# Kernel tuning notes

Measured on AMD Instinct MI355X. Metric: run time of the kernel, lower is better.

Reference implementation:

```python
import jax, jax.numpy as jnp
import numpy as np

H = 2048      # hidden_size
NH = 16       # num attention heads
KVH = 4       # num kv heads (GQA)
D = 128       # head_dim
E = 32        # num experts
K = 4         # top-k experts per token
I = 768       # moe intermediate size
T = 1024      # num tokens (single prefill sequence)
EPS = 1e-6
THETA = 10000.0


def rmsnorm(x, w, eps=EPS):
    return x * jax.lax.rsqrt(jnp.mean(x * x, axis=-1, keepdims=True) + eps) * w


def rope_cos_sin(positions, dim, theta):
    inv_freq = 1.0 / (theta ** (jnp.arange(0, dim, 2, dtype=jnp.float32) / dim))
    freqs = positions.astype(jnp.float32)[:, None] * inv_freq[None, :]   # [T, D/2]
    emb = jnp.concatenate([freqs, freqs], axis=-1)                       # [T, D]
    return jnp.cos(emb), jnp.sin(emb)


def apply_rope(x, cos, sin):
    # x: [T, nH, D]; cos/sin: [T, D] -> neox style: cat(-x2, x1)
    x1, x2 = jnp.split(x, 2, axis=-1)
    x_rot = jnp.concatenate([-x2, x1], axis=-1)
    return cos[:, None, :] * x + sin[:, None, :] * x_rot


def setup_inputs() -> dict:
    key = jax.random.key(0)
    ks = jax.random.split(key, 8)
    s = 0.02
    return {
        "hidden_states": jax.random.normal(ks[0], (T, H), jnp.float32),
        "positions": jnp.arange(T, dtype=jnp.int32),
        "ln1_w": jnp.ones((H,), jnp.float32),
        "w_qkv": jax.random.normal(ks[1], ((NH + 2 * KVH) * D, H), jnp.float32) * s,
        "q_norm_w": jnp.ones((D,), jnp.float32),
        "k_norm_w": jnp.ones((D,), jnp.float32),
        "w_o": jax.random.normal(ks[2], (H, NH * D), jnp.float32) * s,
        "ln2_w": jnp.ones((H,), jnp.float32),
        "router_w": jax.random.normal(ks[3], (E, H), jnp.float32) * s,
        "w_gate": jax.random.normal(ks[4], (E, I, H), jnp.float32) * s,
        "w_up": jax.random.normal(ks[5], (E, I, H), jnp.float32) * s,
        "w_down": jax.random.normal(ks[6], (E, H, I), jnp.float32) * s,
    }


def decoder_layer(hidden_states, positions, ln1_w, w_qkv, q_norm_w, k_norm_w,
                  w_o, ln2_w, router_w, w_gate, w_up, w_down):
    # ---- attention block ----
    residual = hidden_states
    h = rmsnorm(hidden_states, ln1_w)

    qkv = h @ w_qkv.T                                      # [T, (NH+2*KVH)*D]
    q, k, v = jnp.split(qkv, [NH * D, (NH + KVH) * D], axis=-1)
    q = q.reshape(T, NH, D)
    k = k.reshape(T, KVH, D)
    v = v.reshape(T, KVH, D)

    # per-head RMSNorm on q and k (Qwen3 QK-norm)
    q = rmsnorm(q, q_norm_w)
    k = rmsnorm(k, k_norm_w)

    cos, sin = rope_cos_sin(positions, D, THETA)
    q = apply_rope(q, cos, sin)
    k = apply_rope(k, cos, sin)

    rep = NH // KVH
    k = jnp.repeat(k, rep, axis=1)                         # [T, NH, D]
    v = jnp.repeat(v, rep, axis=1)

    scale = D ** -0.5
    scores = jnp.einsum("qhd,khd->hqk", q, k) * scale      # [NH, T, T]
    causal = jnp.tril(jnp.ones((T, T), bool))
    scores = jnp.where(causal[None], scores, -1e30)
    probs = jax.nn.softmax(scores, axis=-1)
    attn = jnp.einsum("hqk,khd->qhd", probs, v).reshape(T, NH * D)
    attn_out = attn @ w_o.T                                # [T, H]

    hidden = residual + attn_out

    # ---- MoE block ----
    residual = hidden
    h = rmsnorm(hidden, ln2_w)

    logits = h @ router_w.T                                # [T, E]
    router_probs = jax.nn.softmax(logits, axis=-1)
    topk_w, topk_idx = jax.lax.top_k(router_probs, K)      # softmax-then-topk
    topk_w = topk_w / (jnp.sum(topk_w, axis=-1, keepdims=True) + 1e-20)

    # scatter top-k weights into a dense [T, E] combine matrix
    combine = jnp.zeros((T, E), h.dtype).at[
        jnp.arange(T)[:, None], topk_idx].add(topk_w)

    gate = jnp.einsum("th,eih->tei", h, w_gate)            # [T, E, I]
    up = jnp.einsum("th,eih->tei", h, w_up)
    act = jax.nn.silu(gate) * up
    moe_out = jnp.einsum("tei,ehi,te->th", act, w_down, combine)

    return residual + moe_out


def reference(hidden_states, positions, ln1_w, w_qkv, q_norm_w, k_norm_w,
              w_o, ln2_w, router_w, w_gate, w_up, w_down):
    return decoder_layer(hidden_states, positions, ln1_w, w_qkv, q_norm_w,
                         k_norm_w, w_o, ln2_w, router_w, w_gate, w_up, w_down)
```

## Files before the change

### kernel.cpp

```cpp
#include <hip/hip_runtime.h>

typedef __attribute__((ext_vector_type(4))) float f32x4;
typedef __attribute__((ext_vector_type(8))) __bf16 bf16x8;
typedef __attribute__((ext_vector_type(4))) __bf16 bf16x4;

__device__ __forceinline__ f32x4 mfma16(bf16x8 a, bf16x8 b, f32x4 c) {
  return __builtin_amdgcn_mfma_f32_16x16x32_bf16(a, b, c, 0, 0, 0);
}

__global__ __launch_bounds__(256) void rmsnorm_k(const float* __restrict__ x,
                                                 const float* __restrict__ w,
                                                 float* __restrict__ y,
                                                 __bf16* __restrict__ yb) {
  int t = blockIdx.x;
  const float* xr = x + (size_t)t * 2048;
  int d0 = threadIdx.x * 4;
  float4 v1 = *(const float4*)(xr + d0);
  float4 v2 = *(const float4*)(xr + 1024 + d0);
  float ss = v1.x*v1.x + v1.y*v1.y + v1.z*v1.z + v1.w*v1.w
           + v2.x*v2.x + v2.y*v2.y + v2.z*v2.z + v2.w*v2.w;
#pragma unroll
  for (int mk = 1; mk < 64; mk <<= 1) ss += __shfl_xor(ss, mk);
  __shared__ float red[4];
  if ((threadIdx.x & 63) == 0) red[threadIdx.x >> 6] = ss;
  __syncthreads();
  float tot = red[0] + red[1] + red[2] + red[3];
  float rs = rsqrtf(tot * (1.0f / 2048.0f) + 1e-6f);
  float* yr = y + (size_t)t * 2048;
  float4 w1 = *(const float4*)(w + d0);
  float4 w2 = *(const float4*)(w + 1024 + d0);
  float4 o1, o2;
  o1.x = v1.x*rs*w1.x; o1.y = v1.y*rs*w1.y; o1.z = v1.z*rs*w1.z; o1.w = v1.w*rs*w1.w;
  o2.x = v2.x*rs*w2.x; o2.y = v2.y*rs*w2.y; o2.z = v2.z*rs*w2.z; o2.w = v2.w*rs*w2.w;
  *(float4*)(yr + d0) = o1;
  *(float4*)(yr + 1024 + d0) = o2;
  if (yb) {
    bf16x4 b1, b2;
    b1[0] = (__bf16)o1.x; b1[1] = (__bf16)o1.y; b1[2] = (__bf16)o1.z; b1[3] = (__bf16)o1.w;
    b2[0] = (__bf16)o2.x; b2[1] = (__bf16)o2.y; b2[2] = (__bf16)o2.z; b2[3] = (__bf16)o2.w;
    *(bf16x4*)(yb + (size_t)t * 2048 + d0) = b1;
    *(bf16x4*)(yb + (size_t)t * 2048 + 1024 + d0) = b2;
  }
}

__global__ __launch_bounds__(256) void gemm3_k(const float* __restrict__ A,
                                               const float* __restrict__ B,
                                               const float* __restrict__ RESID,
                                               float* __restrict__ C, int N, int K) {
  __shared__ __align__(16) __bf16 smAh[128 * 40];
  __shared__ __align__(16) __bf16 smAl[128 * 40];
  __shared__ __align__(16) __bf16 smBh[64 * 40];
  __shared__ __align__(16) __bf16 smBl[64 * 40];
  const int m0 = blockIdx.x * 128, n0 = blockIdx.y * 64;
  const int tid = threadIdx.x, l = tid & 63, w = tid >> 6;
  const int wm = w >> 1, wn = w & 1;
  float4 ra[4], rb[2];
#pragma unroll
  for (int i = 0; i < 4; i++) {
    int c = tid + i * 256, row = c >> 3, k4 = c & 7;
    ra[i] = *(const float4*)(A + (size_t)(m0 + row) * K + k4 * 4);
  }
#pragma unroll
  for (int i = 0; i < 2; i++) {
    int c = tid + i * 256, row = c >> 3, k4 = c & 7;
    rb[i] = *(const float4*)(B + (size_t)(n0 + row) * K + k4 * 4);
  }
  f32x4 acc[4][2] = {};
  for (int kt = 0; kt < K; kt += 32) {
    __syncthreads();
#pragma unroll
    for (int i = 0; i < 4; i++) {
      int c = tid + i * 256, row = c >> 3, k4 = c & 7;
      bf16x4 hv, lv;
#pragma unroll
      for (int j = 0; j < 4; j++) {
        float f = ((const float*)&ra[i])[j];
        __bf16 h = (__bf16)f; hv[j] = h; lv[j] = (__bf16)(f - (float)h);
      }
      *(bf16x4*)(smAh + row * 40 + k4 * 4) = hv;
      *(bf16x4*)(smAl + row * 40 + k4 * 4) = lv;
    }
#pragma unroll
    for (int i = 0; i < 2; i++) {
      int c = tid + i * 256, row = c >> 3, k4 = c & 7;
      bf16x4 hv, lv;
#pragma unroll
      for (int j = 0; j < 4; j++) {
        float f = ((const float*)&rb[i])[j];
        __bf16 h = (__bf16)f; hv[j] = h; lv[j] = (__bf16)(f - (float)h);
      }
      *(bf16x4*)(smBh + row * 40 + k4 * 4) = hv;
      *(bf16x4*)(smBl + row * 40 + k4 * 4) = lv;
    }
    __syncthreads();
    if (kt + 32 < K) {
#pragma unroll
      for (int i = 0; i < 4; i++) {
        int c = tid + i * 256, row = c >> 3, k4 = c & 7;
        ra[i] = *(const float4*)(A + (size_t)(m0 + row) * K + kt + 32 + k4 * 4);
      }
#pragma unroll
      for (int i = 0; i < 2; i++) {
        int c = tid + i * 256, row = c >> 3, k4 = c & 7;
        rb[i] = *(const float4*)(B + (size_t)(n0 + row) * K + kt + 32 + k4 * 4);
      }
    }
    bf16x8 ah[4], al[4], bh[2], bl[2];
    const int ko = (l >> 4) * 8;
#pragma unroll
    for (int f = 0; f < 4; f++) {
      int ar = wm * 64 + f * 16 + (l & 15);
      ah[f] = *(const bf16x8*)(smAh + ar * 40 + ko);
      al[f] = *(const bf16x8*)(smAl + ar * 40 + ko);
    }
#pragma unroll
    for (int f = 0; f < 2; f++) {
      int br = wn * 32 + f * 16 + (l & 15);
      bh[f] = *(const bf16x8*)(smBh + br * 40 + ko);
      bl[f] = *(const bf16x8*)(smBl + br * 40 + ko);
    }
#pragma unroll
    for (int mf = 0; mf < 4; mf++)
#pragma unroll
      for (int nf = 0; nf < 2; nf++) {
        acc[mf][nf] = mfma16(ah[mf], bh[nf], acc[mf][nf]);
        acc[mf][nf] = mfma16(ah[mf], bl[nf], acc[mf][nf]);
        acc[mf][nf] = mfma16(al[mf], bh[nf], acc[mf][nf]);
      }
  }
#pragma unroll
  for (int mf = 0; mf < 4; mf++) {
    int row = m0 + wm * 64 + mf * 16 + ((l >> 4) << 2);
#pragma unroll
    for (int nf = 0; nf < 2; nf++) {
      int col = n0 + wn * 32 + nf * 16 + (l & 15);
#pragma unroll
      for (int r = 0; r < 4; r++) {
        float v = acc[mf][nf][r];
        if (RESID) v += RESID[(size_t)(row + r) * N + col];
        C[(size_t)(row + r) * N + col] = v;
      }
    }
  }
}

__global__ __launch_bounds__(128) void qkr_k(const float* __restrict__ qkv,
                                             const int* __restrict__ pos,
                                             const float* __restrict__ qw,
                                             const float* __restrict__ kw,
                                             __bf16* __restrict__ qh, __bf16* __restrict__ ql,
                                             __bf16* __restrict__ kh, __bf16* __restrict__ kl,
                                             __bf16* __restrict__ vh, __bf16* __restrict__ vl) {
  int hs = blockIdx.x, t = blockIdx.y, d = threadIdx.x;
  float x = qkv[(size_t)t * 3072 + hs * 128 + d];
  __shared__ float xs[128];
  __shared__ float red[2];
  float o;
  if (hs < 20) {
    float ss = x * x;
#pragma unroll
    for (int mk = 1; mk < 64; mk <<= 1) ss += __shfl_xor(ss, mk);
    if ((d & 63) == 0) red[d >> 6] = ss;
    __syncthreads();
    float rs = rsqrtf((red[0] + red[1]) * (1.0f / 128.0f) + 1e-6f);
    const float* w = (hs < 16) ? qw : kw;
    float xn = x * rs * w[d];
    xs[d] = xn;
    __syncthreads();
    int i = d & 63;
    float invf = (float)pow(10000.0, -(double)i / 64.0);
    float ang = (float)pos[t] * invf;
    float cf = (float)cos((double)ang);
    float sf = (float)sin((double)ang);
    float rot = (d < 64) ? -xs[d + 64] : xs[d - 64];
    o = cf * xn + sf * rot;
  } else {
    o = x;
  }
  __bf16 hi = (__bf16)o;
  __bf16 lo = (__bf16)(o - (float)hi);
  if (hs < 16) {
    size_t idx = ((size_t)hs * 1024 + t) * 128 + d;
    qh[idx] = hi; ql[idx] = lo;
  } else if (hs < 20) {
    size_t idx = ((size_t)(hs - 16) * 1024 + t) * 128 + d;
    kh[idx] = hi; kl[idx] = lo;
  } else {
    size_t idx = ((size_t)(hs - 20) * 1024 + t) * 128 + d;
    vh[idx] = hi; vl[idx] = lo;
  }
}

__global__ void vtrans_k(const __bf16* __restrict__ vh, const __bf16* __restrict__ vl,
                         __bf16* __restrict__ vhT, __bf16* __restrict__ vlT) {
  __shared__ __bf16 tile[32][33];
  int kv = blockIdx.z, t0 = blockIdx.x * 32, d0 = blockIdx.y * 32;
  int tx = threadIdx.x, ty = threadIdx.y;
  tile[ty][tx] = vh[((size_t)kv * 1024 + t0 + ty) * 128 + d0 + tx];
  __syncthreads();
  vhT[((size_t)kv * 128 + d0 + ty) * 1024 + t0 + tx] = tile[tx][ty];
  __syncthreads();
  tile[ty][tx] = vl[((size_t)kv * 1024 + t0 + ty) * 128 + d0 + tx];
  __syncthreads();
  vlT[((size_t)kv * 128 + d0 + ty) * 1024 + t0 + tx] = tile[tx][ty];
}

__global__ __launch_bounds__(256) void flash_k(const __bf16* __restrict__ qh, const __bf16* __restrict__ ql,
                                               const __bf16* __restrict__ kh, const __bf16* __restrict__ kl,
                                               const __bf16* __restrict__ vhT, const __bf16* __restrict__ vlT,
                                               float* __restrict__ attn) {
  constexpr int KH = 0, KL = 4352, VH = 8704, VL = 13824, PH = 18944, PL = 21504;
  __shared__ __align__(16) __bf16 sm[24064];
  const int qt = blockIdx.x, h = blockIdx.y;
  const int q0 = qt * 64, kvh = h >> 2;
  const int tid = threadIdx.x, l = tid & 63, w = tid >> 6;
  for (int c = tid; c < 1024; c += 256) {
    int row = c >> 4, dc = c & 15;
    size_t g = ((size_t)h * 1024 + q0 + row) * 128 + dc * 8;
    *(bf16x8*)(sm + row * 136 + dc * 8) = *(const bf16x8*)(qh + g);
    *(bf16x8*)(sm + 8704 + row * 136 + dc * 8) = *(const bf16x8*)(ql + g);
  }
  __syncthreads();
  bf16x8 fqh[4], fql[4];
  {
    int row = w * 16 + (l & 15);
    int ko = (l >> 4) * 8;
#pragma unroll
    for (int kk = 0; kk < 4; kk++) {
      fqh[kk] = *(const bf16x8*)(sm + row * 136 + kk * 32 + ko);
      fql[kk] = *(const bf16x8*)(sm + 8704 + row * 136 + kk * 32 + ko);
    }
  }
  f32x4 acc[8] = {};
  float m_run[4], l_run[4];
#pragma unroll
  for (int r = 0; r < 4; r++) { m_run[r] = -1e30f; l_run[r] = 0.0f; }
  const int ktiles = (q0 + 64) >> 5;
  for (int kt = 0; kt < ktiles; kt++) {
    const int k0 = kt * 32;
    __syncthreads();
    for (int c = tid; c < 512; c += 256) {
      int row = c >> 4, dc = c & 15;
      size_t g = ((size_t)kvh * 1024 + k0 + row) * 128 + dc * 8;
      *(bf16x8*)(sm + KH + row * 136 + dc * 8) = *(const bf16x8*)(kh + g);
      *(bf16x8*)(sm + KL + row * 136 + dc * 8) = *(const bf16x8*)(kl + g);
    }
    for (int c = tid; c < 512; c += 256) {
      int row = c >> 2, tc = c & 3;
      size_t g = ((size_t)kvh * 128 + row) * 1024 + k0 + tc * 8;
      *(bf16x8*)(sm + VH + row * 40 + tc * 8) = *(const bf16x8*)(vhT + g);
      *(bf16x8*)(sm + VL + row * 40 + tc * 8) = *(const bf16x8*)(vlT + g);
    }
    __syncthreads();
    f32x4 s[2] = {};
#pragma unroll
    for (int kk = 0; kk < 4; kk++) {
      int ko = kk * 32 + (l >> 4) * 8;
#pragma unroll
      for (int nf = 0; nf < 2; nf++) {
        int key = nf * 16 + (l & 15);
        bf16x8 bh_ = *(const bf16x8*)(sm + KH + key * 136 + ko);
        bf16x8 bl_ = *(const bf16x8*)(sm + KL + key * 136 + ko);
        s[nf] = mfma16(fqh[kk], bh_, s[nf]);
        s[nf] = mfma16(fqh[kk], bl_, s[nf]);
        s[nf] = mfma16(fql[kk], bh_, s[nf]);
      }
    }
    const float scale = 0.08838834764831845f;
    const bool need_mask = (k0 + 31 > q0);
    float p[2][4], alpha[4];
#pragma unroll
    for (int r = 0; r < 4; r++) {
      float s0 = s[0][r] * scale, s1 = s[1][r] * scale;
      if (need_mask) {
        int qi = q0 + w * 16 + ((l >> 4) << 2) + r;
        if (k0 + (l & 15) > qi) s0 = -1e30f;
        if (k0 + 16 + (l & 15) > qi) s1 = -1e30f;
      }
      float mt = fmaxf(s0, s1);
#pragma unroll
      for (int mk = 1; mk < 16; mk <<= 1) mt = fmaxf(mt, __shfl_xor(mt, mk));
      float mnew = fmaxf(m_run[r], mt);
      alpha[r] = expf(m_run[r] - mnew);
      float p0 = expf(s0 - mnew), p1 = expf(s1 - mnew);
      float rs = p0 + p1;
#pragma unroll
      for (int mk = 1; mk < 16; mk <<= 1) rs += __shfl_xor(rs, mk);
      l_run[r] = l_run[r] * alpha[r] + rs;
      m_run[r] = mnew;
      p[0][r] = p0; p[1][r] = p1;
    }
#pragma unroll
    for (int nf2 = 0; nf2 < 8; nf2++)
#pragma unroll
      for (int r = 0; r < 4; r++) acc[nf2][r] *= alpha[r];
    const int phb = PH + w * 640, plb = PL + w * 640;
#pragma unroll
    for (int nf = 0; nf < 2; nf++)
#pragma unroll
      for (int r = 0; r < 4; r++) {
        int row = ((l >> 4) << 2) + r, col = nf * 16 + (l & 15);
        __bf16 hi = (__bf16)p[nf][r];
        sm[phb + row * 40 + col] = hi;
        sm[plb + row * 40 + col] = (__bf16)(p[nf][r] - (float)hi);
      }
    bf16x8 aph = *(const bf16x8*)(sm + phb + (l & 15) * 40 + (l >> 4) * 8);
    bf16x8 apl = *(const bf16x8*)(sm + plb + (l & 15) * 40 + (l >> 4) * 8);
#pragma unroll
    for (int nf2 = 0; nf2 < 8; nf2++) {
      int drow = nf2 * 16 + (l & 15);
      bf16x8 bvh = *(const bf16x8*)(sm + VH + drow * 40 + (l >> 4) * 8);
      bf16x8 bvl = *(const bf16x8*)(sm + VL + drow * 40 + (l >> 4) * 8);
      acc[nf2] = mfma16(aph, bvh, acc[nf2]);
      acc[nf2] = mfma16(aph, bvl, acc[nf2]);
      acc[nf2] = mfma16(apl, bvh, acc[nf2]);
    }
  }
#pragma unroll
  for (int r = 0; r < 4; r++) {
    float inv = 1.0f / l_run[r];
    size_t t = q0 + w * 16 + ((l >> 4) << 2) + r;
#pragma unroll
    for (int nf2 = 0; nf2 < 8; nf2++)
      attn[t * 2048 + h * 128 + nf2 * 16 + (l & 15)] = acc[nf2][r] * inv;
  }
}

__global__ __launch_bounds__(256) void router_k(const float* __restrict__ h2,
                                                const float* __restrict__ rw,
                                                int* __restrict__ tidx, float* __restrict__ tw,
                                                int* __restrict__ counts) {
  int t = blockIdx.x;
  int e = threadIdx.x >> 3, sub = threadIdx.x & 7;
  const float* hrow = h2 + (size_t)t * 2048;
  const float* wrow = rw + (size_t)e * 2048;
  float acc = 0.0f;
  for (int d = sub * 4; d < 2048; d += 32) {
    float4 a = *(const float4*)(hrow + d);
    float4 b = *(const float4*)(wrow + d);
    acc += a.x * b.x + a.y * b.y + a.z * b.z + a.w * b.w;
  }
  acc += __shfl_xor(acc, 1); acc += __shfl_xor(acc, 2); acc += __shfl_xor(acc, 4);
  __shared__ float lg[32];
  if (sub == 0) lg[e] = acc;
  __syncthreads();
  if (threadIdx.x < 64) {
    int l = threadIdx.x;
    float v = (l < 32) ? lg[l] : -3e38f;
    float mx = v;
#pragma unroll
    for (int mk = 1; mk < 32; mk <<= 1) mx = fmaxf(mx, __shfl_xor(mx, mk));
    float ex = (l < 32) ? expf(v - mx) : 0.0f;
    float den = ex;
#pragma unroll
    for (int mk = 1; mk < 32; mk <<= 1) den += __shfl_xor(den, mk);
    float prob = ex / den;
    float pv = v;
    int sel_i[4]; float sel_w[4]; float wsum = 0.0f;
#pragma unroll
    for (int j = 0; j < 4; j++) {
      float m2 = pv;
#pragma unroll
      for (int mk = 1; mk < 32; mk <<= 1) m2 = fmaxf(m2, __shfl_xor(m2, mk));
      unsigned long long ball = __ballot((pv == m2) && (l < 32));
      int sel = __ffsll(ball) - 1;
      float ps = __shfl(prob, sel);
      sel_i[j] = sel; sel_w[j] = ps; wsum += ps;
      if (l == sel) pv = -3e38f;
    }
    if (l < 4) {
      tidx[t * 4 + l] = sel_i[l];
      tw[t * 4 + l] = sel_w[l] / (wsum + 1e-20f);
      atomicAdd(&counts[sel_i[l]], 1);
    }
  }
}

__global__ void zero_k(int* counts) { if (threadIdx.x < 32) counts[threadIdx.x] = 0; }

__global__ void scan_k(const int* __restrict__ counts, int* __restrict__ offs,
                       int* __restrict__ cursor, int* __restrict__ pair_e,
                       int* __restrict__ pair_mt) {
  int l = threadIdx.x;
  int c = (l < 32) ? counts[l] : 0;
  int x = c;
#pragma unroll
  for (int d = 1; d < 32; d <<= 1) {
    int y = __shfl_up(x, d);
    if (l >= d) x += y;
  }
  if (l < 32) { offs[l] = x - c; cursor[l] = 0; }
  if (l == 31) offs[32] = x;
  if (l == 0) {
    int n = 0;
    for (int e = 0; e < 32; e++) {
      int ce = counts[e];
      for (int m = 0; m * 128 < ce; m++) { pair_e[n] = e; pair_mt[n] = m; n++; }
    }
    for (; n < 64; n++) { pair_e[n] = -1; pair_mt[n] = 0; }
  }
}

__global__ __launch_bounds__(256) void scatter_k(const int* __restrict__ tidx,
                                                 const int* __restrict__ offs,
                                                 int* __restrict__ cursor,
                                                 int* __restrict__ row_of_slot,
                                                 int* __restrict__ tok_of_row) {
  int p = blockIdx.x * 256 + threadIdx.x;
  if (p >= 4096) return;
  int e = tidx[p];
  int pos = atomicAdd(&cursor[e], 1);
  int row = offs[e] + pos;
  row_of_slot[p] = row;
  tok_of_row[row] = p >> 2;
}

__global__ __launch_bounds__(256) void gateup_k(const __bf16* __restrict__ h2b,
                                                const float* __restrict__ wg,
                                                const float* __restrict__ wu,
                                                const int* __restrict__ counts,
                                                const int* __restrict__ offs,
                                                const int* __restrict__ tok_of_row,
                                                const int* __restrict__ pair_e,
                                                const int* __restrict__ pair_mt,
                                                float* __restrict__ gu) {
  const int p = blockIdx.y;
  const int e = pair_e[p];
  if (e < 0) return;
  const int mt = pair_mt[p];
  const int cnt = counts[e];
  const int j = blockIdx.x;
  const float* wsel = (j < 6) ? wg : wu;
  const int n0 = (j < 6 ? j : j - 6) * 128;
  const int gout = (j < 6) ? 0 : 768;
  __shared__ __align__(16) __bf16 smA0[128 * 72];
  __shared__ __align__(16) __bf16 smA1[128 * 72];
  __shared__ __align__(16) __bf16 smB0[128 * 72];
  __shared__ __align__(16) __bf16 smB1[128 * 72];
  __shared__ int toks[128];
  const int tid = threadIdx.x, l = tid & 63, w = tid >> 6;
  const int wm = w >> 1, wn = w & 1;
  if (tid < 128) {
    int r = mt * 128 + tid;
    toks[tid] = (r < cnt) ? tok_of_row[offs[e] + r] : tok_of_row[offs[e]];
  }
  __syncthreads();
  const float* we = wsel + (size_t)e * 768 * 2048;
  const __bf16* aS[4];
  int aD[4];
#pragma unroll
  for (int i = 0; i < 4; i++) {
    aS[i] = h2b + (size_t)toks[(tid >> 3) + 32 * i] * 2048 + (tid & 7) * 8;
    aD[i] = ((tid >> 3) + 32 * i) * 72 + (tid & 7) * 8;
  }
  const float* bS[8];
  int bD[8];
#pragma unroll
  for (int i = 0; i < 8; i++) {
    bS[i] = we + (size_t)(n0 + (tid >> 4) + 16 * i) * 2048 + (tid & 15) * 4;
    bD[i] = ((tid >> 4) + 16 * i) * 72 + (tid & 15) * 4;
  }

  bf16x8 raE[4], raO[4];
  float4 rbE[8], rbO[8];

#define GU_ISSUE_E(kt) do { _Pragma("unroll") \
  for (int i = 0; i < 4; i++) raE[i] = *(const bf16x8*)(aS[i] + (kt)); \
  _Pragma("unroll") \
  for (int i = 0; i < 8; i++) rbE[i] = *(const float4*)(bS[i] + (kt)); } while (0)
#define GU_ISSUE_O(kt) do { _Pragma("unroll") \
  for (int i = 0; i < 4; i++) raO[i] = *(const bf16x8*)(aS[i] + (kt)); \
  _Pragma("unroll") \
  for (int i = 0; i < 8; i++) rbO[i] = *(const float4*)(bS[i] + (kt)); } while (0)
#define CVT4(dst, src) do { bf16x4 hv_; _Pragma("unroll") \
  for (int q_ = 0; q_ < 4; q_++) hv_[q_] = (__bf16)((const float*)&(src))[q_]; \
  *(bf16x4*)(dst) = hv_; } while (0)
#define GU_WRITE_E(smA, smB) do { _Pragma("unroll") \
  for (int i = 0; i < 4; i++) *(bf16x8*)(smA + aD[i]) = raE[i]; \
  _Pragma("unroll") \
  for (int i = 0; i < 8; i++) CVT4(smB + bD[i], rbE[i]); } while (0)
#define GU_WRITE_O(smA, smB) do { _Pragma("unroll") \
  for (int i = 0; i < 4; i++) *(bf16x8*)(smA + aD[i]) = raO[i]; \
  _Pragma("unroll") \
  for (int i = 0; i < 8; i++) CVT4(smB + bD[i], rbO[i]); } while (0)

  GU_ISSUE_E(0);
  GU_ISSUE_O(64);
  GU_WRITE_E(smA0, smB0);
  __syncthreads();

  f32x4 acc[4][4] = {};
  const int afo = (wm * 64 + (l & 15)) * 72 + (l >> 4) * 8;
  const int bfo = (wn * 64 + (l & 15)) * 72 + (l >> 4) * 8;
#define GU_COMPUTE(smA, smB) do { _Pragma("unroll") \
  for (int kk = 0; kk < 2; kk++) { \
    bf16x8 af_[4], bf_[4]; \
    _Pragma("unroll") \
    for (int f = 0; f < 4; f++) { af_[f] = *(const bf16x8*)(smA + afo + kk * 32 + f * 1152); \
                                  bf_[f] = *(const bf16x8*)(smB + bfo + kk * 32 + f * 1152); } \
    _Pragma("unroll") \
    for (int mf = 0; mf < 4; mf++) \
      _Pragma("unroll") \
      for (int nf = 0; nf < 4; nf++) acc[mf][nf] = mfma16(af_[mf], bf_[nf], acc[mf][nf]); } \
} while (0)

  for (int it = 0; it < 32; it += 2) {
    GU_WRITE_O(smA1, smB1);
    if (it + 2 < 32) GU_ISSUE_E((it + 2) * 64);
    GU_COMPUTE(smA0, smB0);
    __syncthreads();
    if (it + 2 < 32) GU_WRITE_E(smA0, smB0);
    if (it + 3 < 32) GU_ISSUE_O((it + 3) * 64);
    GU_COMPUTE(smA1, smB1);
    __syncthreads();
  }
#undef GU_ISSUE_E
#undef GU_ISSUE_O
#undef GU_WRITE_E
#undef GU_WRITE_O
#undef GU_COMPUTE
#undef CVT4
#pragma unroll
  for (int mf = 0; mf < 4; mf++) {
    int rr = mt * 128 + wm * 64 + mf * 16 + ((l >> 4) << 2);
#pragma unroll
    for (int nf = 0; nf < 4; nf++) {
      int col = gout + n0 + wn * 64 + nf * 16 + (l & 15);
#pragma unroll
      for (int r = 0; r < 4; r++)
        if (rr + r < cnt)
          gu[(size_t)(offs[e] + rr + r) * 1536 + col] = acc[mf][nf][r];
    }
  }
}

__global__ __launch_bounds__(192) void silu_k(const float* __restrict__ gu,
                                              __bf16* __restrict__ act) {
  int r = blockIdx.x, c = threadIdx.x * 4;
  float4 g = *(const float4*)(gu + (size_t)r * 1536 + c);
  float4 u = *(const float4*)(gu + (size_t)r * 1536 + 768 + c);
  bf16x4 o;
  o[0] = (__bf16)(g.x / (1.0f + expf(-g.x)) * u.x);
  o[1] = (__bf16)(g.y / (1.0f + expf(-g.y)) * u.y);
  o[2] = (__bf16)(g.z / (1.0f + expf(-g.z)) * u.z);
  o[3] = (__bf16)(g.w / (1.0f + expf(-g.w)) * u.w);
  *(bf16x4*)(act + (size_t)r * 768 + c) = o;
}

__global__ __launch_bounds__(256) void down_k(const __bf16* __restrict__ act,
                                              const float* __restrict__ wd,
                                              const int* __restrict__ counts,
                                              const int* __restrict__ offs,
                                              const int* __restrict__ pair_e,
                                              const int* __restrict__ pair_mt,
                                              float* __restrict__ dout) {
  const int p = blockIdx.y;
  const int e = pair_e[p];
  if (e < 0) return;
  const int mt = pair_mt[p];
  const int cnt = counts[e];
  const int n0 = blockIdx.x * 128;
  __shared__ __align__(16) __bf16 smA0[128 * 72];
  __shared__ __align__(16) __bf16 smA1[128 * 72];
  __shared__ __align__(16) __bf16 smB0[128 * 72];
  __shared__ __align__(16) __bf16 smB1[128 * 72];
  const int tid = threadIdx.x, l = tid & 63, w = tid >> 6;
  const int wm = w >> 1, wn = w & 1;
  const float* wde = wd + (size_t)e * 2048 * 768;
  const int base = offs[e] + mt * 128;
  const __bf16* aS[4];
  int aD[4];
#pragma unroll
  for (int i = 0; i < 4; i++) {
    int rg = base + (tid >> 3) + 32 * i; if (rg > 4095) rg = 4095;
    aS[i] = act + (size_t)rg * 768 + (tid & 7) * 8;
    aD[i] = ((tid >> 3) + 32 * i) * 72 + (tid & 7) * 8;
  }
  const float* bS[8];
  int bD[8];
#pragma unroll
  for (int i = 0; i < 8; i++) {
    bS[i] = wde + (size_t)(n0 + (tid >> 4) + 16 * i) * 768 + (tid & 15) * 4;
    bD[i] = ((tid >> 4) + 16 * i) * 72 + (tid & 15) * 4;
  }

  bf16x8 raE[4], raO[4];
  float4 rbE[8], rbO[8];

#define DN_ISSUE_E(kt) do { _Pragma("unroll") \
  for (int i = 0; i < 4; i++) raE[i] = *(const bf16x8*)(aS[i] + (kt)); \
  _Pragma("unroll") \
  for (int i = 0; i < 8; i++) rbE[i] = *(const float4*)(bS[i] + (kt)); } while (0)
#define DN_ISSUE_O(kt) do { _Pragma("unroll") \
  for (int i = 0; i < 4; i++) raO[i] = *(const bf16x8*)(aS[i] + (kt)); \
  _Pragma("unroll") \
  for (int i = 0; i < 8; i++) rbO[i] = *(const float4*)(bS[i] + (kt)); } while (0)
#define CVT4(dst, src) do { bf16x4 hv_; _Pragma("unroll") \
  for (int q_ = 0; q_ < 4; q_++) hv_[q_] = (__bf16)((const float*)&(src))[q_]; \
  *(bf16x4*)(dst) = hv_; } while (0)
#define DN_WRITE_E(smA, smB) do { _Pragma("unroll") \
  for (int i = 0; i < 4; i++) *(bf16x8*)(smA + aD[i]) = raE[i]; \
  _Pragma("unroll") \
  for (int i = 0; i < 8; i++) CVT4(smB + bD[i], rbE[i]); } while (0)
#define DN_WRITE_O(smA, smB) do { _Pragma("unroll") \
  for (int i = 0; i < 4; i++) *(bf16x8*)(smA + aD[i]) = raO[i]; \
  _Pragma("unroll") \
  for (int i = 0; i < 8; i++) CVT4(smB + bD[i], rbO[i]); } while (0)

  DN_ISSUE_E(0);
  DN_ISSUE_O(64);
  DN_WRITE_E(smA0, smB0);
  __syncthreads();

  f32x4 acc[4][4] = {};
  const int afo = (wm * 64 + (l & 15)) * 72 + (l >> 4) * 8;
  const int bfo = (wn * 64 + (l & 15)) * 72 + (l >> 4) * 8;
#define DN_COMPUTE(smA, smB) do { _Pragma("unroll") \
  for (int kk = 0; kk < 2; kk++) { \
    bf16x8 af_[4], bf_[4]; \
    _Pragma("unroll") \
    for (int f = 0; f < 4; f++) { af_[f] = *(const bf16x8*)(smA + afo + kk * 32 + f * 1152); \
                                  bf_[f] = *(const bf16x8*)(smB + bfo + kk * 32 + f * 1152); } \
    _Pragma("unroll") \
    for (int mf = 0; mf < 4; mf++) \
      _Pragma("unroll") \
      for (int nf = 0; nf < 4; nf++) acc[mf][nf] = mfma16(af_[mf], bf_[nf], acc[mf][nf]); } \
} while (0)

  for (int it = 0; it < 12; it += 2) {
    DN_WRITE_O(smA1, smB1);
    if (it + 2 < 12) DN_ISSUE_E((it + 2) * 64);
    DN_COMPUTE(smA0, smB0);
    __syncthreads();
    if (it + 2 < 12) DN_WRITE_E(smA0, smB0);
    if (it + 3 < 12) DN_ISSUE_O((it + 3) * 64);
    DN_COMPUTE(smA1, smB1);
    __syncthreads();
  }
#undef DN_ISSUE_E
#undef DN_ISSUE_O
#undef DN_WRITE_E
#undef DN_WRITE_O
#undef DN_COMPUTE
#undef CVT4
#pragma unroll
  for (int mf = 0; mf < 4; mf++) {
    int rr = mt * 128 + wm * 64 + mf * 16 + ((l >> 4) << 2);
#pragma unroll
    for (int nf = 0; nf < 4; nf++) {
      int col = n0 + wn * 64 + nf * 16 + (l & 15);
#pragma unroll
      for (int r = 0; r < 4; r++)
        if (rr + r < cnt)
          dout[(size_t)(offs[e] + rr + r) * 2048 + col] = acc[mf][nf][r];
    }
  }
}

__global__ __launch_bounds__(256) void combine_k(const float* __restrict__ hidden,
                                                 const float* __restrict__ dout,
                                                 const int* __restrict__ row_of_slot,
                                                 const float* __restrict__ tw,
                                                 float* __restrict__ out) {
  int t = blockIdx.x;
  int r0 = row_of_slot[t * 4 + 0], r1 = row_of_slot[t * 4 + 1];
  int r2 = row_of_slot[t * 4 + 2], r3 = row_of_slot[t * 4 + 3];
  float w0 = tw[t * 4 + 0], w1 = tw[t * 4 + 1], w2 = tw[t * 4 + 2], w3 = tw[t * 4 + 3];
  const float* h = hidden + (size_t)t * 2048;
  float* o = out + (size_t)t * 2048;
  for (int d = threadIdx.x * 4; d < 2048; d += 1024) {
    float4 hv = *(const float4*)(h + d);
    float4 a0 = *(const float4*)(dout + (size_t)r0 * 2048 + d);
    float4 a1 = *(const float4*)(dout + (size_t)r1 * 2048 + d);
    float4 a2 = *(const float4*)(dout + (size_t)r2 * 2048 + d);
    float4 a3 = *(const float4*)(dout + (size_t)r3 * 2048 + d);
    float4 ov;
    ov.x = hv.x + w0 * a0.x + w1 * a1.x + w2 * a2.x + w3 * a3.x;
    ov.y = hv.y + w0 * a0.y + w1 * a1.y + w2 * a2.y + w3 * a3.y;
    ov.z = hv.z + w0 * a0.z + w1 * a1.z + w2 * a2.z + w3 * a3.z;
    ov.w = hv.w + w0 * a0.w + w1 * a1.w + w2 * a2.w + w3 * a3.w;
    *(float4*)(o + d) = ov;
  }
}

extern "C" void kernel_launch(void* const* d_in, const int* in_sizes, int n_in,
                              void* d_out, int out_size, void* d_ws, size_t ws_size,
                              hipStream_t stream) {
  (void)in_sizes; (void)n_in; (void)out_size; (void)ws_size;
  const float* hs   = (const float*)d_in[0];
  const int*   pos  = (const int*)d_in[1];
  const float* ln1w = (const float*)d_in[2];
  const float* wqkv = (const float*)d_in[3];
  const float* qnw  = (const float*)d_in[4];
  const float* knw  = (const float*)d_in[5];
  const float* wo   = (const float*)d_in[6];
  const float* ln2w = (const float*)d_in[7];
  const float* rw   = (const float*)d_in[8];
  const float* wg   = (const float*)d_in[9];
  const float* wu   = (const float*)d_in[10];
  const float* wd   = (const float*)d_in[11];
  float* out = (float*)d_out;
  char* ws = (char*)d_ws;

  float*  h1     = (float*)(ws + 0);
  float*  gu     = (float*)(ws + 0);
  float*  dout   = (float*)(ws + 0);
  float*  qkv    = (float*)(ws + 8388608);
  __bf16* qh     = (__bf16*)(ws + 20971520);
  __bf16* ql     = (__bf16*)(ws + 25165824);
  __bf16* kh     = (__bf16*)(ws + 29360128);
  __bf16* kl     = (__bf16*)(ws + 30408704);
  __bf16* vh     = (__bf16*)(ws + 31457280);
  __bf16* vl     = (__bf16*)(ws + 32505856);
  __bf16* vhT    = (__bf16*)(ws + 33554432);
  __bf16* vlT    = (__bf16*)(ws + 34603008);
  int*    pair_e = (int*)(ws + 33554432);
  int*    pair_mt= (int*)(ws + 33554944);
  float*  attn   = (float*)(ws + 35651584);
  __bf16* h2b    = (__bf16*)(ws + 35651584);
  __bf16* act    = (__bf16*)(ws + 35651584);
  float*  hidden = (float*)(ws + 44040192);
  float*  h2     = (float*)(ws + 52428800);
  int*    tidx   = (int*)(ws + 60817408);
  float*  tw     = (float*)(ws + 60833792);
  int*    counts = (int*)(ws + 60850176);
  int*    offs   = (int*)(ws + 60850432);
  int*    cursor = (int*)(ws + 60850688);
  int*    row_of_slot = (int*)(ws + 60850944);
  int*    tok_of_row  = (int*)(ws + 60867328);

  rmsnorm_k<<<1024, 256, 0, stream>>>(hs, ln1w, h1, nullptr);
  gemm3_k<<<dim3(8, 48), 256, 0, stream>>>(h1, wqkv, nullptr, qkv, 3072, 2048);
  qkr_k<<<dim3(24, 1024), 128, 0, stream>>>(qkv, pos, qnw, knw, qh, ql, kh, kl, vh, vl);
  vtrans_k<<<dim3(32, 4, 4), dim3(32, 32), 0, stream>>>(vh, vl, vhT, vlT);
  flash_k<<<dim3(16, 16), 256, 0, stream>>>(qh, ql, kh, kl, vhT, vlT, attn);
  gemm3_k<<<dim3(8, 32), 256, 0, stream>>>(attn, wo, hs, hidden, 2048, 2048);

  rmsnorm_k<<<1024, 256, 0, stream>>>(hidden, ln2w, h2, h2b);
  zero_k<<<1, 64, 0, stream>>>(counts);
  router_k<<<1024, 256, 0, stream>>>(h2, rw, tidx, tw, counts);
  scan_k<<<1, 64, 0, stream>>>(counts, offs, cursor, pair_e, pair_mt);
  scatter_k<<<16, 256, 0, stream>>>(tidx, offs, cursor, row_of_slot, tok_of_row);
  gateup_k<<<dim3(12, 64), 256, 0, stream>>>(h2b, wg, wu, counts, offs, tok_of_row, pair_e, pair_mt, gu);
  silu_k<<<4096, 192, 0, stream>>>(gu, act);
  down_k<<<dim3(16, 64), 256, 0, stream>>>(act, wd, counts, offs, pair_e, pair_mt, dout);
  combine_k<<<1024, 256, 0, stream>>>(hidden, dout, row_of_slot, tw, out);
}
```

Before: 561.4 us.

## Double-buffer LDS in the split-bf16 GEMM and halve MoE expert M-tiles

The dense split-bf16 GEMM used for QKV and the output projection now keeps two LDS buffers. It issues global loads for the next k-tile while MFMA runs on the current one, so there is only one barrier per tile. The MoE gate/up and down kernels switch from 128-row to 64-row token tiles per expert, with the scan producing up to 96 (expert, tile) pairs and a larger grid. This cuts padding waste on partially filled tiles and raises the block count. The cost is that each expert's fp32 weights are read and converted by more blocks, and the dense GEMM uses twice the LDS, which may lower occupancy.

```diff
diff --git a/kernel.cpp b/kernel.cpp
--- a/kernel.cpp
+++ b/kernel.cpp
@@ -47,87 +47,94 @@
                                                const float* __restrict__ B,
                                                const float* __restrict__ RESID,
                                                float* __restrict__ C, int N, int K) {
-  __shared__ __align__(16) __bf16 smAh[128 * 40];
-  __shared__ __align__(16) __bf16 smAl[128 * 40];
-  __shared__ __align__(16) __bf16 smBh[64 * 40];
-  __shared__ __align__(16) __bf16 smBl[64 * 40];
+  __shared__ __align__(16) __bf16 smAh0[128 * 40];
+  __shared__ __align__(16) __bf16 smAl0[128 * 40];
+  __shared__ __align__(16) __bf16 smBh0[64 * 40];
+  __shared__ __align__(16) __bf16 smBl0[64 * 40];
+  __shared__ __align__(16) __bf16 smAh1[128 * 40];
+  __shared__ __align__(16) __bf16 smAl1[128 * 40];
+  __shared__ __align__(16) __bf16 smBh1[64 * 40];
+  __shared__ __align__(16) __bf16 smBl1[64 * 40];
   const int m0 = blockIdx.x * 128, n0 = blockIdx.y * 64;
   const int tid = threadIdx.x, l = tid & 63, w = tid >> 6;
   const int wm = w >> 1, wn = w & 1;
-  float4 ra[4], rb[2];
+  const float* aS[4]; const float* bS[2];
+  int aD[4], bD[2];
 #pragma unroll
   for (int i = 0; i < 4; i++) {
-    int c = tid + i * 256, row = c >> 3, k4 = c & 7;
-    ra[i] = *(const float4*)(A + (size_t)(m0 + row) * K + k4 * 4);
+    aS[i] = A + (size_t)(m0 + (tid >> 3) + 32 * i) * K + (tid & 7) * 4;
+    aD[i] = ((tid >> 3) + 32 * i) * 40 + (tid & 7) * 4;
   }
 #pragma unroll
   for (int i = 0; i < 2; i++) {
-    int c = tid + i * 256, row = c >> 3, k4 = c & 7;
-    rb[i] = *(const float4*)(B + (size_t)(n0 + row) * K + k4 * 4);
-  }
+    bS[i] = B + (size_t)(n0 + (tid >> 3) + 32 * i) * K + (tid & 7) * 4;
+    bD[i] = ((tid >> 3) + 32 * i) * 40 + (tid & 7) * 4;
+  }
+  float4 raE[4], rbE[2], raO[4], rbO[2];
+
+#define GE_ISSUE_E(kt) do { _Pragma("unroll") \
+  for (int i = 0; i < 4; i++) raE[i] = *(const float4*)(aS[i] + (kt)); \
+  _Pragma("unroll") \
+  for (int i = 0; i < 2; i++) rbE[i] = *(const float4*)(bS[i] + (kt)); } while (0)
+#define GE_ISSUE_O(kt) do { _Pragma("unroll") \
+  for (int i = 0; i < 4; i++) raO[i] = *(const float4*)(aS[i] + (kt)); \
+  _Pragma("unroll") \
+  for (int i = 0; i < 2; i++) rbO[i] = *(const float4*)(bS[i] + (kt)); } while (0)
+#define SPLIT4(dh, dl, src) do { bf16x4 hv_, lv_; _Pragma("unroll") \
+  for (int q_ = 0; q_ < 4; q_++) { float f_ = ((const float*)&(src))[q_]; \
+    __bf16 h_ = (__bf16)f_; hv_[q_] = h_; lv_[q_] = (__bf16)(f_ - (float)h_); } \
+  *(bf16x4*)(dh) = hv_; *(bf16x4*)(dl) = lv_; } while (0)
+#define GE_WRITE_E(sAh, sAl, sBh, sBl) do { _Pragma("unroll") \
+  for (int i = 0; i < 4; i++) SPLIT4(sAh + aD[i], sAl + aD[i], raE[i]); \
+  _Pragma("unroll") \
+  for (int i = 0; i < 2; i++) SPLIT4(sBh + bD[i], sBl + bD[i], rbE[i]); } while (0)
+#define GE_WRITE_O(sAh, sAl, sBh, sBl) do { _Pragma("unroll") \
+  for (int i = 0; i < 4; i++) SPLIT4(sAh + aD[i], sAl + aD[i], raO[i]); \
+  _Pragma("unroll") \
+  for (int i = 0; i < 2; i++) SPLIT4(sBh + bD[i], sBl + bD[i], rbO[i]); } while (0)
+
+  GE_ISSUE_E(0);
+  GE_ISSUE_O(32);
+  GE_WRITE_E(smAh0, smAl0, smBh0, smBl0);
+  __syncthreads();
+
   f32x4 acc[4][2] = {};
-  for (int kt = 0; kt < K; kt += 32) {
-    __syncthreads();
-#pragma unroll
-    for (int i = 0; i < 4; i++) {
-      int c = tid + i * 256, row = c >> 3, k4 = c & 7;
-      bf16x4 hv, lv;
-#pragma unroll
-      for (int j = 0; j < 4; j++) {
-        float f = ((const float*)&ra[i])[j];
-        __bf16 h = (__bf16)f; hv[j] = h; lv[j] = (__bf16)(f - (float)h);
-      }
-      *(bf16x4*)(smAh + row * 40 + k4 * 4) = hv;
-      *(bf16x4*)(smAl + row * 40 + k4 * 4) = lv;
-    }
-#pragma unroll
-    for (int i = 0; i < 2; i++) {
-      int c = tid + i * 256, row = c >> 3, k4 = c & 7;
-      bf16x4 hv, lv;
-#pragma unroll
-      for (int j = 0; j < 4; j++) {
-        float f = ((const float*)&rb[i])[j];
-        __bf16 h = (__bf16)f; hv[j] = h; lv[j] = (__bf16)(f - (float)h);
-      }
-      *(bf16x4*)(smBh + row * 40 + k4 * 4) = hv;
-      *(bf16x4*)(smBl + row * 40 + k4 * 4) = lv;
-    }
-    __syncthreads();
-    if (kt + 32 < K) {
-#pragma unroll
-      for (int i = 0; i < 4; i++) {
-        int c = tid + i * 256, row = c >> 3, k4 = c & 7;
-        ra[i] = *(const float4*)(A + (size_t)(m0 + row) * K + kt + 32 + k4 * 4);
-      }
-#pragma unroll
-      for (int i = 0; i < 2; i++) {
-        int c = tid + i * 256, row = c >> 3, k4 = c & 7;
-        rb[i] = *(const float4*)(B + (size_t)(n0 + row) * K + kt + 32 + k4 * 4);
-      }
-    }
-    bf16x8 ah[4], al[4], bh[2], bl[2];
-    const int ko = (l >> 4) * 8;
-#pragma unroll
-    for (int f = 0; f < 4; f++) {
-      int ar = wm * 64 + f * 16 + (l & 15);
-      ah[f] = *(const bf16x8*)(smAh + ar * 40 + ko);
-      al[f] = *(const bf16x8*)(smAl + ar * 40 + ko);
-    }
-#pragma unroll
-    for (int f = 0; f < 2; f++) {
-      int br = wn * 32 + f * 16 + (l & 15);
-      bh[f] = *(const bf16x8*)(smBh + br * 40 + ko);
-      bl[f] = *(const bf16x8*)(smBl + br * 40 + ko);
-    }
-#pragma unroll
-    for (int mf = 0; mf < 4; mf++)
-#pragma unroll
-      for (int nf = 0; nf < 2; nf++) {
-        acc[mf][nf] = mfma16(ah[mf], bh[nf], acc[mf][nf]);
-        acc[mf][nf] = mfma16(ah[mf], bl[nf], acc[mf][nf]);
-        acc[mf][nf] = mfma16(al[mf], bh[nf], acc[mf][nf]);
-      }
-  }
+  const int afo = (wm * 64 + (l & 15)) * 40 + (l >> 4) * 8;
+  const int bfo = (wn * 32 + (l & 15)) * 40 + (l >> 4) * 8;
+#define GE_COMPUTE(sAh, sAl, sBh, sBl) do { \
+  bf16x8 ah_[4], al_[4], bh_[2], bl_[2]; \
+  _Pragma("unroll") \
+  for (int f = 0; f < 4; f++) { ah_[f] = *(const bf16x8*)(sAh + afo + f * 640); \
+                                al_[f] = *(const bf16x8*)(sAl + afo + f * 640); } \
+  _Pragma("unroll") \
+  for (int f = 0; f < 2; f++) { bh_[f] = *(const bf16x8*)(sBh + bfo + f * 640); \
+                                bl_[f] = *(const bf16x8*)(sBl + bfo + f * 640); } \
+  _Pragma("unroll") \
+  for (int mf = 0; mf < 4; mf++) \
+    _Pragma("unroll") \
+    for (int nf = 0; nf < 2; nf++) { \
+      acc[mf][nf] = mfma16(ah_[mf], bh_[nf], acc[mf][nf]); \
+      acc[mf][nf] = mfma16(ah_[mf], bl_[nf], acc[mf][nf]); \
+      acc[mf][nf] = mfma16(al_[mf], bh_[nf], acc[mf][nf]); } \
+} while (0)
+
+  const int ntiles = K >> 5;
+  for (int it = 0; it < ntiles; it += 2) {
+    GE_WRITE_O(smAh1, smAl1, smBh1, smBl1);
+    if (it + 2 < ntiles) GE_ISSUE_E((it + 2) * 32);
+    GE_COMPUTE(smAh0, smAl0, smBh0, smBl0);
+    __syncthreads();
+    if (it + 2 < ntiles) GE_WRITE_E(smAh0, smAl0, smBh0, smBl0);
+    if (it + 3 < ntiles) GE_ISSUE_O((it + 3) * 32);
+    GE_COMPUTE(smAh1, smAl1, smBh1, smBl1);
+    __syncthreads();
+  }
+#undef GE_ISSUE_E
+#undef GE_ISSUE_O
+#undef GE_WRITE_E
+#undef GE_WRITE_O
+#undef GE_COMPUTE
+#undef SPLIT4
 #pragma unroll
   for (int mf = 0; mf < 4; mf++) {
     int row = m0 + wm * 64 + mf * 16 + ((l >> 4) << 2);
@@ -395,9 +402,9 @@
     int n = 0;
     for (int e = 0; e < 32; e++) {
       int ce = counts[e];
-      for (int m = 0; m * 128 < ce; m++) { pair_e[n] = e; pair_mt[n] = m; n++; }
-    }
-    for (; n < 64; n++) { pair_e[n] = -1; pair_mt[n] = 0; }
+      for (int m = 0; m * 64 < ce && n < 96; m++) { pair_e[n] = e; pair_mt[n] = m; n++; }
+    }
+    for (; n < 96; n++) { pair_e[n] = -1; pair_mt[n] = 0; }
   }
 }
 
@@ -433,23 +440,22 @@
   const float* wsel = (j < 6) ? wg : wu;
   const int n0 = (j < 6 ? j : j - 6) * 128;
   const int gout = (j < 6) ? 0 : 768;
-  __shared__ __align__(16) __bf16 smA0[128 * 72];
-  __shared__ __align__(16) __bf16 smA1[128 * 72];
+  __shared__ __align__(16) __bf16 smA0[64 * 72];
+  __shared__ __align__(16) __bf16 smA1[64 * 72];
   __shared__ __align__(16) __bf16 smB0[128 * 72];
   __shared__ __align__(16) __bf16 smB1[128 * 72];
-  __shared__ int toks[128];
+  __shared__ int toks[64];
   const int tid = threadIdx.x, l = tid & 63, w = tid >> 6;
-  const int wm = w >> 1, wn = w & 1;
-  if (tid < 128) {
-    int r = mt * 128 + tid;
+  if (tid < 64) {
+    int r = mt * 64 + tid;
     toks[tid] = (r < cnt) ? tok_of_row[offs[e] + r] : tok_of_row[offs[e]];
   }
   __syncthreads();
   const float* we = wsel + (size_t)e * 768 * 2048;
-  const __bf16* aS[4];
-  int aD[4];
-#pragma unroll
-  for (int i = 0; i < 4; i++) {
+  const __bf16* aS[2];
+  int aD[2];
+#pragma unroll
+  for (int i = 0; i < 2; i++) {
     aS[i] = h2b + (size_t)toks[(tid >> 3) + 32 * i] * 2048 + (tid & 7) * 8;
     aD[i] = ((tid >> 3) + 32 * i) * 72 + (tid & 7) * 8;
   }
@@ -461,26 +467,26 @@
     bD[i] = ((tid >> 4) + 16 * i) * 72 + (tid & 15) * 4;
   }
 
-  bf16x8 raE[4], raO[4];
+  bf16x8 raE[2], raO[2];
   float4 rbE[8], rbO[8];
 
 #define GU_ISSUE_E(kt) do { _Pragma("unroll") \
-  for (int i = 0; i < 4; i++) raE[i] = *(const bf16x8*)(aS[i] + (kt)); \
+  for (int i = 0; i < 2; i++) raE[i] = *(const bf16x8*)(aS[i] + (kt)); \
   _Pragma("unroll") \
   for (int i = 0; i < 8; i++) rbE[i] = *(const float4*)(bS[i] + (kt)); } while (0)
 #define GU_ISSUE_O(kt) do { _Pragma("unroll") \
-  for (int i = 0; i < 4; i++) raO[i] = *(const bf16x8*)(aS[i] + (kt)); \
+  for (int i = 0; i < 2; i++) raO[i] = *(const bf16x8*)(aS[i] + (kt)); \
   _Pragma("unroll") \
   for (int i = 0; i < 8; i++) rbO[i] = *(const float4*)(bS[i] + (kt)); } while (0)
 #define CVT4(dst, src) do { bf16x4 hv_; _Pragma("unroll") \
   for (int q_ = 0; q_ < 4; q_++) hv_[q_] = (__bf16)((const float*)&(src))[q_]; \
   *(bf16x4*)(dst) = hv_; } while (0)
 #define GU_WRITE_E(smA, smB) do { _Pragma("unroll") \
-  for (int i = 0; i < 4; i++) *(bf16x8*)(smA + aD[i]) = raE[i]; \
+  for (int i = 0; i < 2; i++) *(bf16x8*)(smA + aD[i]) = raE[i]; \
   _Pragma("unroll") \
   for (int i = 0; i < 8; i++) CVT4(smB + bD[i], rbE[i]); } while (0)
 #define GU_WRITE_O(smA, smB) do { _Pragma("unroll") \
-  for (int i = 0; i < 4; i++) *(bf16x8*)(smA + aD[i]) = raO[i]; \
+  for (int i = 0; i < 2; i++) *(bf16x8*)(smA + aD[i]) = raO[i]; \
   _Pragma("unroll") \
   for (int i = 0; i < 8; i++) CVT4(smB + bD[i], rbO[i]); } while (0)
 
@@ -489,19 +495,20 @@
   GU_WRITE_E(smA0, smB0);
   __syncthreads();
 
-  f32x4 acc[4][4] = {};
-  const int afo = (wm * 64 + (l & 15)) * 72 + (l >> 4) * 8;
-  const int bfo = (wn * 64 + (l & 15)) * 72 + (l >> 4) * 8;
+  f32x4 acc[4][2] = {};
+  const int afo = ((l & 15)) * 72 + (l >> 4) * 8;
+  const int bfo = (w * 32 + (l & 15)) * 72 + (l >> 4) * 8;
 #define GU_COMPUTE(smA, smB) do { _Pragma("unroll") \
   for (int kk = 0; kk < 2; kk++) { \
-    bf16x8 af_[4], bf_[4]; \
+    bf16x8 af_[4], bf_[2]; \
     _Pragma("unroll") \
-    for (int f = 0; f < 4; f++) { af_[f] = *(const bf16x8*)(smA + afo + kk * 32 + f * 1152); \
-                                  bf_[f] = *(const bf16x8*)(smB + bfo + kk * 32 + f * 1152); } \
+    for (int f = 0; f < 4; f++) af_[f] = *(const bf16x8*)(smA + afo + kk * 32 + f * 1152); \
+    _Pragma("unroll") \
+    for (int f = 0; f < 2; f++) bf_[f] = *(const bf16x8*)(smB + bfo + kk * 32 + f * 1152); \
     _Pragma("unroll") \
     for (int mf = 0; mf < 4; mf++) \
       _Pragma("unroll") \
-      for (int nf = 0; nf < 4; nf++) acc[mf][nf] = mfma16(af_[mf], bf_[nf], acc[mf][nf]); } \
+      for (int nf = 0; nf < 2; nf++) acc[mf][nf] = mfma16(af_[mf], bf_[nf], acc[mf][nf]); } \
 } while (0)
 
   for (int it = 0; it < 32; it += 2) {
@@ -522,10 +529,10 @@
 #undef CVT4
 #pragma unroll
   for (int mf = 0; mf < 4; mf++) {
-    int rr = mt * 128 + wm * 64 + mf * 16 + ((l >> 4) << 2);
-#pragma unroll
-    for (int nf = 0; nf < 4; nf++) {
-      int col = gout + n0 + wn * 64 + nf * 16 + (l & 15);
+    int rr = mt * 64 + mf * 16 + ((l >> 4) << 2);
+#pragma unroll
+    for (int nf = 0; nf < 2; nf++) {
+      int col = gout + n0 + w * 32 + nf * 16 + (l & 15);
 #pragma unroll
       for (int r = 0; r < 4; r++)
         if (rr + r < cnt)
@@ -560,18 +567,17 @@
   const int mt = pair_mt[p];
   const int cnt = counts[e];
   const int n0 = blockIdx.x * 128;
-  __shared__ __align__(16) __bf16 smA0[128 * 72];
-  __shared__ __align__(16) __bf16 smA1[128 * 72];
+  __shared__ __align__(16) __bf16 smA0[64 * 72];
+  __shared__ __align__(16) __bf16 smA1[64 * 72];
   __shared__ __align__(16) __bf16 smB0[128 * 72];
   __shared__ __align__(16) __bf16 smB1[128 * 72];
   const int tid = threadIdx.x, l = tid & 63, w = tid >> 6;
-  const int wm = w >> 1, wn = w & 1;
   const float* wde = wd + (size_t)e * 2048 * 768;
-  const int base = offs[e] + mt * 128;
-  const __bf16* aS[4];
-  int aD[4];
-#pragma unroll
-  for (int i = 0; i < 4; i++) {
+  const int base = offs[e] + mt * 64;
+  const __bf16* aS[2];
+  int aD[2];
+#pragma unroll
+  for (int i = 0; i < 2; i++) {
     int rg = base + (tid >> 3) + 32 * i; if (rg > 4095) rg = 4095;
     aS[i] = act + (size_t)rg * 768 + (tid & 7) * 8;
     aD[i] = ((tid >> 3) + 32 * i) * 72 + (tid & 7) * 8;
@@ -584,26 +590,26 @@
     bD[i] = ((tid >> 4) + 16 * i) * 72 + (tid & 15) * 4;
   }
 
-  bf16x8 raE[4], raO[4];
+  bf16x8 raE[2], raO[2];
   float4 rbE[8], rbO[8];
 
 #define DN_ISSUE_E(kt) do { _Pragma("unroll") \
-  for (int i = 0; i < 4; i++) raE[i] = *(const bf16x8*)(aS[i] + (kt)); \
+  for (int i = 0; i < 2; i++) raE[i] = *(const bf16x8*)(aS[i] + (kt)); \
   _Pragma("unroll") \
   for (int i = 0; i < 8; i++) rbE[i] = *(const float4*)(bS[i] + (kt)); } while (0)
 #define DN_ISSUE_O(kt) do { _Pragma("unroll") \
-  for (int i = 0; i < 4; i++) raO[i] = *(const bf16x8*)(aS[i] + (kt)); \
+  for (int i = 0; i < 2; i++) raO[i] = *(const bf16x8*)(aS[i] + (kt)); \
   _Pragma("unroll") \
   for (int i = 0; i < 8; i++) rbO[i] = *(const float4*)(bS[i] + (kt)); } while (0)
 #define CVT4(dst, src) do { bf16x4 hv_; _Pragma("unroll") \
   for (int q_ = 0; q_ < 4; q_++) hv_[q_] = (__bf16)((const float*)&(src))[q_]; \
   *(bf16x4*)(dst) = hv_; } while (0)
 #define DN_WRITE_E(smA, smB) do { _Pragma("unroll") \
-  for (int i = 0; i < 4; i++) *(bf16x8*)(smA + aD[i]) = raE[i]; \
+  for (int i = 0; i < 2; i++) *(bf16x8*)(smA + aD[i]) = raE[i]; \
   _Pragma("unroll") \
   for (int i = 0; i < 8; i++) CVT4(smB + bD[i], rbE[i]); } while (0)
 #define DN_WRITE_O(smA, smB) do { _Pragma("unroll") \
-  for (int i = 0; i < 4; i++) *(bf16x8*)(smA + aD[i]) = raO[i]; \
+  for (int i = 0; i < 2; i++) *(bf16x8*)(smA + aD[i]) = raO[i]; \
   _Pragma("unroll") \
   for (int i = 0; i < 8; i++) CVT4(smB + bD[i], rbO[i]); } while (0)
 
@@ -612,19 +618,20 @@
   DN_WRITE_E(smA0, smB0);
   __syncthreads();
 
-  f32x4 acc[4][4] = {};
-  const int afo = (wm * 64 + (l & 15)) * 72 + (l >> 4) * 8;
-  const int bfo = (wn * 64 + (l & 15)) * 72 + (l >> 4) * 8;
+  f32x4 acc[4][2] = {};
+  const int afo = ((l & 15)) * 72 + (l >> 4) * 8;
+  const int bfo = (w * 32 + (l & 15)) * 72 + (l >> 4) * 8;
 #define DN_COMPUTE(smA, smB) do { _Pragma("unroll") \
   for (int kk = 0; kk < 2; kk++) { \
-    bf16x8 af_[4], bf_[4]; \
+    bf16x8 af_[4], bf_[2]; \
     _Pragma("unroll") \
-    for (int f = 0; f < 4; f++) { af_[f] = *(const bf16x8*)(smA + afo + kk * 32 + f * 1152); \
-                                  bf_[f] = *(const bf16x8*)(smB + bfo + kk * 32 + f * 1152); } \
+    for (int f = 0; f < 4; f++) af_[f] = *(const bf16x8*)(smA + afo + kk * 32 + f * 1152); \
+    _Pragma("unroll") \
+    for (int f = 0; f < 2; f++) bf_[f] = *(const bf16x8*)(smB + bfo + kk * 32 + f * 1152); \
     _Pragma("unroll") \
     for (int mf = 0; mf < 4; mf++) \
       _Pragma("unroll") \
-      for (int nf = 0; nf < 4; nf++) acc[mf][nf] = mfma16(af_[mf], bf_[nf], acc[mf][nf]); } \
+      for (int nf = 0; nf < 2; nf++) acc[mf][nf] = mfma16(af_[mf], bf_[nf], acc[mf][nf]); } \
 } while (0)
 
   for (int it = 0; it < 12; it += 2) {
@@ -645,10 +652,10 @@
 #undef CVT4
 #pragma unroll
   for (int mf = 0; mf < 4; mf++) {
-    int rr = mt * 128 + wm * 64 + mf * 16 + ((l >> 4) << 2);
-#pragma unroll
-    for (int nf = 0; nf < 4; nf++) {
-      int col = n0 + wn * 64 + nf * 16 + (l & 15);
+    int rr = mt * 64 + mf * 16 + ((l >> 4) << 2);
+#pragma unroll
+    for (int nf = 0; nf < 2; nf++) {
+      int col = n0 + w * 32 + nf * 16 + (l & 15);
 #pragma unroll
       for (int r = 0; r < 4; r++)
         if (rr + r < cnt)
@@ -741,8 +748,8 @@
   router_k<<<1024, 256, 0, stream>>>(h2, rw, tidx, tw, counts);
   scan_k<<<1, 64, 0, stream>>>(counts, offs, cursor, pair_e, pair_mt);
   scatter_k<<<16, 256, 0, stream>>>(tidx, offs, cursor, row_of_slot, tok_of_row);
-  gateup_k<<<dim3(12, 64), 256, 0, stream>>>(h2b, wg, wu, counts, offs, tok_of_row, pair_e, pair_mt, gu);
+  gateup_k<<<dim3(12, 96), 256, 0, stream>>>(h2b, wg, wu, counts, offs, tok_of_row, pair_e, pair_mt, gu);
   silu_k<<<4096, 192, 0, stream>>>(gu, act);
-  down_k<<<dim3(16, 64), 256, 0, stream>>>(act, wd, counts, offs, pair_e, pair_mt, dout);
+  down_k<<<dim3(16, 96), 256, 0, stream>>>(act, wd, counts, offs, pair_e, pair_mt, dout);
   combine_k<<<1024, 256, 0, stream>>>(hidden, dout, row_of_slot, tw, out);
 }
```

Measured after the change: 546.9 us, median of 2. 2.6% less time.
